# Kernel optimization log

Measured on AMD Instinct MI355X. Metric: run time of the kernel, lower is better.

## Reference

```python
import jax, jax.numpy as jnp
import numpy as np
from jax import lax

SEQ_LEN = 12
E = 64        # embedding_dim
HD = 128      # h_dim
G = 32        # number of scenes (seq_start_end rows)
P = 32        # pedestrians per scene
B = G * P     # total batch
BOT = 1024    # bottleneck_dim
MLP = 1024    # mlp_dim
BN_S = 1.0 / np.sqrt(1.0 + 1e-5)  # eval BatchNorm1d with running mean 0 / var 1


def setup_inputs():
    key = jax.random.key(0)
    ks = jax.random.split(key, 32)
    r = lambda k, s, sc=0.1: (jax.random.normal(k, s, jnp.float32) * sc)
    starts = np.arange(G, dtype=np.int32) * P
    sse = jnp.asarray(np.stack([starts, starts + P], 1))
    return {
        'last_pos': r(ks[0], (B, 2), 1.0),
        'last_pos_rel': r(ks[1], (B, 2), 1.0),
        'h0': r(ks[2], (1, B, HD), 1.0),
        'c0': r(ks[3], (1, B, HD), 1.0),
        'vx': r(ks[4], (8, B), 1.0),
        'vy': r(ks[5], (8, B), 1.0),
        'agent_type': jax.random.uniform(ks[6], (8, B, 1), jnp.float32),
        'seq_start_end': sse,
        # decoder params
        'W_sp': r(ks[7], (2, E)), 'b_sp': r(ks[8], (E,)),
        'W_ih': r(ks[9], (E, 4 * HD)), 'W_hh': r(ks[10], (HD, 4 * HD)),
        'b_ih': r(ks[11], (4 * HD,)), 'b_hh': r(ks[12], (4 * HD,)),
        'W_h2p': r(ks[13], (HD, 2)), 'b_h2p': r(ks[14], (2,)),
        # AttenPoolNet params
        'Wp_sp': r(ks[15], (2, E)), 'bp_sp': r(ks[16], (E,)),
        'Wp_vel': r(ks[17], (2, E)), 'bp_vel': r(ks[18], (E,)),
        'Wp_at': r(ks[19], (6, E)), 'bp_at': r(ks[20], (E,)),
        'Wa1': r(ks[21], (E, MLP)), 'ba1': r(ks[22], (MLP,)),
        'Wa2': r(ks[23], (MLP, 1)), 'ba2': r(ks[24], (1,)),
        'Wm1': r(ks[25], (E + HD, 512)), 'bm1': r(ks[26], (512,)),
        'Wm2': r(ks[27], (512, BOT)), 'bm2': r(ks[28], (BOT,)),
        # decoder post-pool mlp: [h+bottleneck, mlp_dim, h]
        'Wd1': r(ks[29], (HD + BOT, MLP)), 'bd1': r(ks[30], (MLP,)),
        'Wd2': r(ks[31], (MLP, HD)), 'bd2': jnp.zeros((HD,), jnp.float32),
    }


def _bnrelu(x):
    # make_mlp: Linear -> BatchNorm1d (eval, mean 0 / var 1) -> ReLU
    return jax.nn.relu(x * BN_S)


def reference(last_pos, last_pos_rel, h0, c0, vx, vy, agent_type, seq_start_end,
              W_sp, b_sp, W_ih, W_hh, b_ih, b_hh, W_h2p, b_h2p,
              Wp_sp, bp_sp, Wp_vel, bp_vel, Wp_at, bp_at,
              Wa1, ba1, Wa2, ba2, Wm1, bm1, Wm2, bm2,
              Wd1, bd1, Wd2, bd2):
    g = seq_start_end.shape[0]
    p = last_pos.shape[0] // g

    at0 = agent_type[0].reshape(g, p, 1)               # agent_type[0,:,:] per group
    at_rep = jnp.repeat(at0, 6, axis=-1)               # .repeat(num_ped, 6) width expansion
    at_emb = at_rep @ Wp_at + bp_at                    # (g,p,E), index j (tiled over i)
    vel = jnp.stack([vx[-1], vy[-1]], -1).reshape(g, p, 2)
    _vel_emb = vel @ Wp_vel + bp_vel                   # computed in source, unused downstream

    def pool(h2d, pos):
        Hh = h2d.reshape(g, p, HD)
        pg = pos.reshape(g, p, 2)
        # rel[s,i,j] = pos[s,j] - pos[s,i]
        rel = pg[:, None, :, :] - pg[:, :, None, :]
        rel_emb = rel @ Wp_sp + bp_sp                  # (g,p,p,E)
        a = _bnrelu(rel_emb @ Wa1 + ba1)               # (g,p,p,MLP)
        s = _bnrelu(a @ Wa2 + ba2)                     # (g,p,p,1)
        w = jax.nn.softmax(s, axis=-1)                 # torch softmax(dim=1) over size-1 axis -> ones
        base = jnp.concatenate([Hh, at_emb], -1)       # (g,p,192), index j
        wt = base[:, None, :, :] * (0.05 * w)          # (g,p,p,192)
        m = _bnrelu(wt @ Wm1 + bm1)
        m = _bnrelu(m @ Wm2 + bm2)                     # (g,p,p,BOT)
        return m.max(axis=2).reshape(g * p, BOT)       # max over j per tile index i

    def lstm(x, h, c):
        gates = x @ W_ih + h @ W_hh + b_ih + b_hh
        i, f, gg, o = jnp.split(gates, 4, axis=-1)
        c = jax.nn.sigmoid(f) * c + jax.nn.sigmoid(i) * jnp.tanh(gg)
        h = jax.nn.sigmoid(o) * jnp.tanh(c)
        return h, c

    def step(carry, _):
        lp, di, h, c = carry
        h, c = lstm(di, h, c)
        rel = h @ W_h2p + b_h2p
        cur = rel + lp
        ph = pool(h, cur)
        dh = _bnrelu(jnp.concatenate([h, ph], -1) @ Wd1 + bd1)
        dh = _bnrelu(dh @ Wd2 + bd2)
        di = rel @ W_sp + b_sp
        return (cur, di, dh, c), rel

    init = (last_pos, last_pos_rel @ W_sp + b_sp, h0[0], c0[0])
    (lp, di, h, c), rels = lax.scan(step, init, None, length=SEQ_LEN)
    return rels, h[None]  # (seq_len,B,2), (1,B,HD)
```

## Files before the change

### kernel.cpp

```cpp
#include <hip/hip_runtime.h>
#include <math.h>

#define BN_SF 0.9999950000374997f

typedef __attribute__((ext_vector_type(8))) short short8v;
typedef __attribute__((ext_vector_type(4))) float float4v;

__device__ __forceinline__ float sigm(float x) { return 1.0f / (1.0f + expf(-x)); }

__device__ __forceinline__ short f2bf(float x) {
    unsigned u = __builtin_bit_cast(unsigned, x);
    unsigned r = (u + 0x7fffu + ((u >> 16) & 1u)) >> 16;
    return (short)r;
}
__device__ __forceinline__ float bf2f(short h) {
    unsigned u = ((unsigned)(unsigned short)h) << 16;
    return __builtin_bit_cast(float, u);
}

template <int K, int N>
__device__ __forceinline__ void cvtB8(const float* __restrict__ src, short* __restrict__ dst,
                                      float scale, int g) {
    const int KCN = K >> 5;
    int ntg = g / (KCN * 64);
    int rem = g - ntg * (KCN * 64);
    int kc = rem >> 6, lane = rem & 63;
    int n = ntg * 16 + (lane & 15);
    int k0 = kc * 32 + ((lane >> 4) << 3);
    short8v v;
#pragma unroll
    for (int j = 0; j < 8; ++j) v[j] = f2bf(scale * src[(size_t)(k0 + j) * N + n]);
    *(short8v*)(dst + (size_t)g * 8) = v;
}

struct SetupP {
    const float *Wm2, *Wd1, *Wd2, *Wm1, *Wih, *Whh, *Wpat, *bpat, *bm1;
    const float *lpr, *Wsp, *bsp, *c0;
    short *Wm2s, *Wd1f, *Wd2f, *Wm1f, *WgHi, *WgLo;
    float *uv, *di, *cbuf;
};

__global__ __launch_bounds__(256) void k_setup(SetupP p) {
    int gt = blockIdx.x * 256 + threadIdx.x;
    int stride = gridDim.x * 256;
    for (int g = gt; g < 512 * 1024 / 8; g += stride)  cvtB8<512, 1024>(p.Wm2, p.Wm2s, 1.f, g);
    for (int g = gt; g < 1152 * 1024 / 8; g += stride) cvtB8<1152, 1024>(p.Wd1, p.Wd1f, 1.f, g);
    for (int g = gt; g < 1024 * 128 / 8; g += stride)  cvtB8<1024, 128>(p.Wd2, p.Wd2f, 1.f, g);
    for (int g = gt; g < 128 * 512 / 8; g += stride)   cvtB8<128, 512>(p.Wm1, p.Wm1f, 0.05f, g);
    for (int g = gt; g < 192 * 512 / 8; g += stride) {
        int ntg = g / (6 * 64);
        int rem = g - ntg * (6 * 64);
        int kc = rem >> 6, lane = rem & 63;
        int n = ntg * 16 + (lane & 15);
        int k0 = kc * 32 + ((lane >> 4) << 3);
        short8v vh, vl;
#pragma unroll
        for (int j = 0; j < 8; ++j) {
            int k = k0 + j;
            float v = (k < 64) ? p.Wih[(size_t)k * 512 + n] : p.Whh[(size_t)(k - 64) * 512 + n];
            short hi = f2bf(v);
            vh[j] = hi; vl[j] = f2bf(v - bf2f(hi));
        }
        *(short8v*)(p.WgHi + (size_t)g * 8) = vh;
        *(short8v*)(p.WgLo + (size_t)g * 8) = vl;
    }
    for (int i = gt; i < 1024 * 64; i += stride) {
        int r = i >> 6, c = i & 63;
        p.di[i] = p.lpr[r * 2] * p.Wsp[c] + p.lpr[r * 2 + 1] * p.Wsp[64 + c] + p.bsp[c];
    }
    for (int i = gt; i < 1024 * 128; i += stride) p.cbuf[i] = p.c0[i];
    if (blockIdx.x == 0) {
        __shared__ float rw[64];
        int t = threadIdx.x;
        if (t < 64) { float s = 0.f; for (int k = 0; k < 6; ++k) s += p.Wpat[k * 64 + t]; rw[t] = s; }
        __syncthreads();
        for (int c = t; c < 512; c += 256) {
            float u = 0.f, v = 0.f;
            for (int e = 0; e < 64; ++e) {
                float wg = p.Wm1[(128 + e) * 512 + c];
                u += rw[e] * wg; v += p.bpat[e] * wg;
            }
            p.uv[c] = 0.05f * u; p.uv[512 + c] = 0.05f * v + p.bm1[c];
        }
    }
}

__global__ __launch_bounds__(512, 4) void k_step(
    const short* __restrict__ WgHi, const short* __restrict__ WgLo,
    const short* __restrict__ Wm1f, const short* __restrict__ Wd2f,
    const short* __restrict__ Wd1f,
    const float* __restrict__ bih, const float* __restrict__ bhh,
    const float* __restrict__ Whp, const float* __restrict__ bhp,
    const float* __restrict__ Wsp, const float* __restrict__ bsp,
    const float* __restrict__ bd1, const float* __restrict__ bd2,
    const float* __restrict__ at0, const float* __restrict__ uv,
    const float* __restrict__ h0,
    const float* __restrict__ phwp, const short* __restrict__ hf_in, int first,
    float* __restrict__ cbuf, float* __restrict__ di,
    short* __restrict__ hf_out, short* __restrict__ m1s,
    float* __restrict__ outrel) {
    __shared__ float sgu[16 * 512];
    __shared__ float sh[16][128];
    __shared__ float sdi[16][64];
    __shared__ float phws[1024];
    __shared__ short xfh[6 * 512];
    __shared__ short xfl[6 * 512];
    __shared__ short xm[4 * 512];
    __shared__ float sat[16];
    __shared__ float srel[16][2];
    short* dh1L = (short*)sgu;
    float* sg = sgu;

    int t = threadIdx.x, b = blockIdx.x;
    int l = t & 63, w = t >> 6;
    int s = b >> 1, mt = b & 1, r0 = b * 16;
    int rbase = (l >> 4) << 2;

    for (int i = t; i < 16 * 64; i += 512) sdi[i >> 6][i & 63] = di[r0 * 64 + i];
    if (t < 16) sat[t] = at0[r0 + t];

    if (first) {
        for (int i = t; i < 16 * 128; i += 512) sh[i >> 7][i & 127] = h0[r0 * 128 + i];
        __syncthreads();
    } else {
        for (int i = t; i < 1024; i += 512) {
            float v = bd1[i];
#pragma unroll
            for (int ct = 0; ct < 8; ++ct) v += phwp[(size_t)s * 8192 + ct * 1024 + i];
            phws[i] = v;
        }
        __syncthreads();
        short8v Ah[4];
#pragma unroll
        for (int kc = 0; kc < 4; ++kc)
            Ah[kc] = *(const short8v*)(hf_in + (size_t)b * 2048 + kc * 512 + l * 8);
#pragma unroll 1
        for (int q2 = 0; q2 < 4; ++q2) {
            short8v B[2][4];
#pragma unroll
            for (int qq = 0; qq < 2; ++qq)
#pragma unroll
                for (int kc = 0; kc < 4; ++kc)
                    B[qq][kc] = *(const short8v*)(Wd1f + (size_t)(w * 8 + q2 * 2 + qq) * 18432 + kc * 512 + l * 8);
            float4v acc2[2];
#pragma unroll
            for (int qq = 0; qq < 2; ++qq) {
                int col = (w * 8 + q2 * 2 + qq) * 16 + (l & 15);
                float pv = phws[col];
                acc2[qq] = (float4v){pv, pv, pv, pv};
            }
#pragma unroll
            for (int kc = 0; kc < 4; ++kc)
#pragma unroll
                for (int qq = 0; qq < 2; ++qq)
                    acc2[qq] = __builtin_amdgcn_mfma_f32_16x16x32_bf16(Ah[kc], B[qq][kc], acc2[qq], 0, 0, 0);
#pragma unroll
            for (int qq = 0; qq < 2; ++qq) {
                int col = (w * 8 + q2 * 2 + qq) * 16 + (l & 15);
                int kcD = col >> 5, jD = col & 7, lD = ((col & 31) >> 3) << 4;
#pragma unroll
                for (int r = 0; r < 4; ++r) {
                    float v = fmaxf(BN_SF * acc2[qq][r], 0.f);
                    dh1L[kcD * 512 + (rbase + r + lD) * 8 + jD] = f2bf(v);
                }
            }
        }
        __syncthreads();
        float4v hacc = {0.f, 0.f, 0.f, 0.f};
        const short* ap = dh1L + l * 8;
        const short* bp = Wd2f + (size_t)w * 16384 + l * 8;
#pragma unroll 1
        for (int kt = 0; kt < 4; ++kt) {
            short8v B[8], A[8];
#pragma unroll
            for (int kk = 0; kk < 8; ++kk) B[kk] = *(const short8v*)(bp + (kt * 8 + kk) * 512);
#pragma unroll
            for (int kk = 0; kk < 8; ++kk) A[kk] = *(const short8v*)(ap + (kt * 8 + kk) * 512);
#pragma unroll
            for (int kk = 0; kk < 8; ++kk)
                hacc = __builtin_amdgcn_mfma_f32_16x16x32_bf16(A[kk], B[kk], hacc, 0, 0, 0);
        }
        int col = w * 16 + (l & 15);
        float bb2 = bd2[col];
        __syncthreads();
#pragma unroll
        for (int r = 0; r < 4; ++r)
            sh[rbase + r][col] = fmaxf(BN_SF * (hacc[r] + bb2), 0.f);
        __syncthreads();
    }

    for (int i = t; i < 6 * 512; i += 512) {
        int pos = i & 511, kc = i >> 9;
        int ll = pos >> 3, j = pos & 7;
        int row = ll & 15, k = kc * 32 + ((ll >> 4) << 3) + j;
        float v = (k < 64) ? sdi[row][k] : sh[row][k - 64];
        short hi = f2bf(v);
        xfh[i] = hi;
        xfl[i] = f2bf(v - bf2f(hi));
    }
    __syncthreads();

    {
        float4v ga[4] = {{0,0,0,0},{0,0,0,0},{0,0,0,0},{0,0,0,0}};
#pragma unroll 1
        for (int kt = 0; kt < 3; ++kt) {
            short8v BH[2][4], BL[2][4], AH[2], AL[2];
#pragma unroll
            for (int kk = 0; kk < 2; ++kk) {
                int kc = kt * 2 + kk;
#pragma unroll
                for (int q = 0; q < 4; ++q) {
                    int nf = w * 4 + q;
                    BH[kk][q] = *(const short8v*)(WgHi + (size_t)nf * 3072 + kc * 512 + l * 8);
                    BL[kk][q] = *(const short8v*)(WgLo + (size_t)nf * 3072 + kc * 512 + l * 8);
                }
                AH[kk] = *(const short8v*)(&xfh[kc * 512 + l * 8]);
                AL[kk] = *(const short8v*)(&xfl[kc * 512 + l * 8]);
            }
#pragma unroll
            for (int kk = 0; kk < 2; ++kk)
#pragma unroll
                for (int q = 0; q < 4; ++q) {
                    ga[q] = __builtin_amdgcn_mfma_f32_16x16x32_bf16(AH[kk], BH[kk][q], ga[q], 0, 0, 0);
                    ga[q] = __builtin_amdgcn_mfma_f32_16x16x32_bf16(AH[kk], BL[kk][q], ga[q], 0, 0, 0);
                    ga[q] = __builtin_amdgcn_mfma_f32_16x16x32_bf16(AL[kk], BH[kk][q], ga[q], 0, 0, 0);
                }
        }
#pragma unroll
        for (int q = 0; q < 4; ++q) {
            int col = (w * 4 + q) * 16 + (l & 15);
            float bb = bih[col] + bhh[col];
#pragma unroll
            for (int r = 0; r < 4; ++r)
                sg[(rbase + r) * 512 + col] = ga[q][r] + bb;
        }
    }
    __syncthreads();

    for (int i = t; i < 16 * 128; i += 512) {
        int row = i >> 7, j = i & 127;
        float gi = sg[row * 512 + j], gf = sg[row * 512 + j + 128];
        float gg = sg[row * 512 + j + 256], go = sg[row * 512 + j + 384];
        float cn = sigm(gf) * cbuf[(r0 + row) * 128 + j] + sigm(gi) * tanhf(gg);
        float hn = sigm(go) * tanhf(cn);
        cbuf[(r0 + row) * 128 + j] = cn;
        sh[row][j] = hn;
    }
    __syncthreads();

    if (t < 32) {
        int row = t >> 1, d = t & 1;
        float s2 = bhp[d];
        for (int k = 0; k < 128; ++k) s2 += sh[row][k] * Whp[k * 2 + d];
        srel[row][d] = s2;
        outrel[(r0 + row) * 2 + d] = s2;
    }
    for (int i = t; i < 4 * 512; i += 512) {
        int pos = i & 511, kc = i >> 9;
        int ll = pos >> 3, j = pos & 7;
        int row = ll & 15, k = kc * 32 + ((ll >> 4) << 3) + j;
        short hv = f2bf(sh[row][k]);
        xm[i] = hv;
        hf_out[(size_t)b * 2048 + i] = hv;
    }
    __syncthreads();

    for (int i = t; i < 16 * 64; i += 512) {
        int row = i >> 6, c = i & 63;
        di[(r0 + row) * 64 + c] = srel[row][0] * Wsp[c] + srel[row][1] * Wsp[64 + c] + bsp[c];
    }

    {
        float4v ma[4] = {{0,0,0,0},{0,0,0,0},{0,0,0,0},{0,0,0,0}};
        short8v A[4], B[4][4];
#pragma unroll
        for (int kc = 0; kc < 4; ++kc) {
#pragma unroll
            for (int q = 0; q < 4; ++q)
                B[kc][q] = *(const short8v*)(Wm1f + (size_t)(w * 4 + q) * 2048 + kc * 512 + l * 8);
            A[kc] = *(const short8v*)(&xm[kc * 512 + l * 8]);
        }
#pragma unroll
        for (int kc = 0; kc < 4; ++kc)
#pragma unroll
            for (int q = 0; q < 4; ++q)
                ma[q] = __builtin_amdgcn_mfma_f32_16x16x32_bf16(A[kc], B[kc][q], ma[q], 0, 0, 0);
#pragma unroll
        for (int q = 0; q < 4; ++q) {
            int col = (w * 4 + q) * 16 + (l & 15);
            float uc = uv[col], vc = uv[512 + col];
#pragma unroll
            for (int r = 0; r < 4; ++r) {
                int rowC = rbase + r;
                float m1v = fmaxf(BN_SF * (ma[q][r] + sat[rowC] * uc + vc), 0.f);
                int kcD = col >> 5;
                int laneD = rowC + (((col & 31) >> 3) << 4);
                m1s[(size_t)s * 16384 + kcD * 1024 + mt * 512 + laneD * 8 + (col & 7)] = f2bf(m1v);
            }
        }
    }
}

__global__ __launch_bounds__(512, 4) void k_m2(const short* __restrict__ m1s,
                                               const short* __restrict__ Wm2s,
                                               const short* __restrict__ Wd1f,
                                               const float* __restrict__ bm2,
                                               float* __restrict__ phwp) {
    __shared__ short sphb[128];
    int t = threadIdx.x, l = t & 63, w = t >> 6;
    int s = blockIdx.x >> 3, ct = blockIdx.x & 7;

    {
        int nf = ct * 8 + w;
        const short* ap = m1s + (size_t)s * 16384 + l * 8;
        const short* bp = Wm2s + (size_t)nf * 8192 + l * 8;
        float4v acc0 = {0,0,0,0}, acc1 = {0,0,0,0};
#pragma unroll 1
        for (int kt = 0; kt < 4; ++kt) {
            short8v A0[4], A1[4], B[4];
#pragma unroll
            for (int kk = 0; kk < 4; ++kk) {
                int kc = kt * 4 + kk;
                B[kk] = *(const short8v*)(bp + kc * 512);
                A0[kk] = *(const short8v*)(ap + kc * 1024);
                A1[kk] = *(const short8v*)(ap + kc * 1024 + 512);
            }
#pragma unroll
            for (int kk = 0; kk < 4; ++kk) {
                acc0 = __builtin_amdgcn_mfma_f32_16x16x32_bf16(A0[kk], B[kk], acc0, 0, 0, 0);
                acc1 = __builtin_amdgcn_mfma_f32_16x16x32_bf16(A1[kk], B[kk], acc1, 0, 0, 0);
            }
        }
        float m = acc0[0];
#pragma unroll
        for (int ri = 1; ri < 4; ++ri) m = fmaxf(m, acc0[ri]);
#pragma unroll
        for (int ri = 0; ri < 4; ++ri) m = fmaxf(m, acc1[ri]);
        m = fmaxf(m, __shfl_xor(m, 16, 64));
        m = fmaxf(m, __shfl_xor(m, 32, 64));
        if (l < 16) {
            int col = nf * 16 + l;
            sphb[w * 16 + l] = f2bf(fmaxf(BN_SF * (m + bm2[col]), 0.f));
        }
    }
    __syncthreads();

    {
        short8v Ap[4];
#pragma unroll
        for (int kk = 0; kk < 4; ++kk)
            Ap[kk] = *(const short8v*)(sphb + kk * 32 + ((l >> 4) << 3));
#pragma unroll 1
        for (int q2 = 0; q2 < 4; ++q2) {
            short8v B[2][4];
#pragma unroll
            for (int qq = 0; qq < 2; ++qq)
#pragma unroll
                for (int kk = 0; kk < 4; ++kk)
                    B[qq][kk] = *(const short8v*)(Wd1f + (size_t)(w * 8 + q2 * 2 + qq) * 18432
                                                  + (size_t)(4 + ct * 4 + kk) * 512 + l * 8);
            float4v acc2[2] = {{0,0,0,0},{0,0,0,0}};
#pragma unroll
            for (int kk = 0; kk < 4; ++kk)
#pragma unroll
                for (int qq = 0; qq < 2; ++qq)
                    acc2[qq] = __builtin_amdgcn_mfma_f32_16x16x32_bf16(Ap[kk], B[qq][kk], acc2[qq], 0, 0, 0);
            if (l < 16) {
#pragma unroll
                for (int qq = 0; qq < 2; ++qq) {
                    int nf_p = w * 8 + q2 * 2 + qq;
                    phwp[(size_t)s * 8192 + ct * 1024 + nf_p * 16 + l] = acc2[qq][0];
                }
            }
        }
    }
}

__global__ __launch_bounds__(512, 4) void k_hfin(const short* __restrict__ Wd2f,
                                                 const short* __restrict__ Wd1f,
                                                 const float* __restrict__ bd1,
                                                 const float* __restrict__ bd2,
                                                 const float* __restrict__ phwp,
                                                 const short* __restrict__ hf,
                                                 float* __restrict__ outh) {
    __shared__ float phws[1024];
    __shared__ short dh1L[16384];
    int t = threadIdx.x, b = blockIdx.x;
    int l = t & 63, w = t >> 6;
    int s = b >> 1, rbase = (l >> 4) << 2;

    for (int i = t; i < 1024; i += 512) {
        float v = bd1[i];
#pragma unroll
        for (int ct = 0; ct < 8; ++ct) v += phwp[(size_t)s * 8192 + ct * 1024 + i];
        phws[i] = v;
    }
    __syncthreads();
    short8v Ah[4];
#pragma unroll
    for (int kc = 0; kc < 4; ++kc)
        Ah[kc] = *(const short8v*)(hf + (size_t)b * 2048 + kc * 512 + l * 8);
#pragma unroll 1
    for (int q2 = 0; q2 < 4; ++q2) {
        short8v B[2][4];
#pragma unroll
        for (int qq = 0; qq < 2; ++qq)
#pragma unroll
            for (int kc = 0; kc < 4; ++kc)
                B[qq][kc] = *(const short8v*)(Wd1f + (size_t)(w * 8 + q2 * 2 + qq) * 18432 + kc * 512 + l * 8);
        float4v acc2[2];
#pragma unroll
        for (int qq = 0; qq < 2; ++qq) {
            int col = (w * 8 + q2 * 2 + qq) * 16 + (l & 15);
            float pv = phws[col];
            acc2[qq] = (float4v){pv, pv, pv, pv};
        }
#pragma unroll
        for (int kc = 0; kc < 4; ++kc)
#pragma unroll
            for (int qq = 0; qq < 2; ++qq)
                acc2[qq] = __builtin_amdgcn_mfma_f32_16x16x32_bf16(Ah[kc], B[qq][kc], acc2[qq], 0, 0, 0);
#pragma unroll
        for (int qq = 0; qq < 2; ++qq) {
            int col = (w * 8 + q2 * 2 + qq) * 16 + (l & 15);
            int kcD = col >> 5, jD = col & 7, lD = ((col & 31) >> 3) << 4;
#pragma unroll
            for (int r = 0; r < 4; ++r) {
                float v = fmaxf(BN_SF * acc2[qq][r], 0.f);
                dh1L[kcD * 512 + (rbase + r + lD) * 8 + jD] = f2bf(v);
            }
        }
    }
    __syncthreads();
    float4v hacc = {0.f, 0.f, 0.f, 0.f};
    const short* ap = dh1L + l * 8;
    const short* bp = Wd2f + (size_t)w * 16384 + l * 8;
#pragma unroll 1
    for (int kt = 0; kt < 4; ++kt) {
        short8v B[8], A[8];
#pragma unroll
        for (int kk = 0; kk < 8; ++kk) B[kk] = *(const short8v*)(bp + (kt * 8 + kk) * 512);
#pragma unroll
        for (int kk = 0; kk < 8; ++kk) A[kk] = *(const short8v*)(ap + (kt * 8 + kk) * 512);
#pragma unroll
        for (int kk = 0; kk < 8; ++kk)
            hacc = __builtin_amdgcn_mfma_f32_16x16x32_bf16(A[kk], B[kk], hacc, 0, 0, 0);
    }
    int col = w * 16 + (l & 15);
    float bb2 = bd2[col];
#pragma unroll
    for (int r = 0; r < 4; ++r)
        outh[(b * 16 + rbase + r) * 128 + col] = fmaxf(BN_SF * (hacc[r] + bb2), 0.f);
}

extern "C" void kernel_launch(void* const* d_in, const int* in_sizes, int n_in,
                              void* d_out, int out_size, void* d_ws, size_t ws_size,
                              hipStream_t stream) {
    const float* last_pos_rel = (const float*)d_in[1];
    const float* h0           = (const float*)d_in[2];
    const float* c0           = (const float*)d_in[3];
    const float* agent_type   = (const float*)d_in[6];
    const float* W_sp  = (const float*)d_in[8];
    const float* b_sp  = (const float*)d_in[9];
    const float* W_ih  = (const float*)d_in[10];
    const float* W_hh  = (const float*)d_in[11];
    const float* b_ih  = (const float*)d_in[12];
    const float* b_hh  = (const float*)d_in[13];
    const float* W_h2p = (const float*)d_in[14];
    const float* b_h2p = (const float*)d_in[15];
    const float* Wp_at = (const float*)d_in[20];
    const float* bp_at = (const float*)d_in[21];
    const float* Wm1   = (const float*)d_in[26];
    const float* bm1   = (const float*)d_in[27];
    const float* Wm2   = (const float*)d_in[28];
    const float* bm2   = (const float*)d_in[29];
    const float* Wd1   = (const float*)d_in[30];
    const float* bd1   = (const float*)d_in[31];
    const float* Wd2   = (const float*)d_in[32];
    const float* bd2   = (const float*)d_in[33];
    float* out = (float*)d_out;

    float* ws   = (float*)d_ws;
    float* uv   = ws;
    float* di   = uv + 1024;
    float* cbuf = di + 65536;
    float* phwp = cbuf + 131072;
    short* hf   = (short*)(phwp + 262144);
    short* m1s  = hf + 131072;
    short* Wm2s = m1s + 524288;
    short* Wd1f = Wm2s + 524288;
    short* Wd2f = Wd1f + 1179648;
    short* Wm1f = Wd2f + 131072;
    short* WgHi = Wm1f + 65536;
    short* WgLo = WgHi + 98304;

    SetupP sp;
    sp.Wm2 = Wm2; sp.Wd1 = Wd1; sp.Wd2 = Wd2; sp.Wm1 = Wm1;
    sp.Wih = W_ih; sp.Whh = W_hh; sp.Wpat = Wp_at; sp.bpat = bp_at; sp.bm1 = bm1;
    sp.lpr = last_pos_rel; sp.Wsp = W_sp; sp.bsp = b_sp; sp.c0 = c0;
    sp.Wm2s = Wm2s; sp.Wd1f = Wd1f; sp.Wd2f = Wd2f;
    sp.Wm1f = Wm1f; sp.WgHi = WgHi; sp.WgLo = WgLo;
    sp.uv = uv; sp.di = di; sp.cbuf = cbuf;

    k_setup<<<2048, 256, 0, stream>>>(sp);

    for (int t = 0; t < 12; ++t) {
        k_step<<<64, 512, 0, stream>>>(WgHi, WgLo, Wm1f, Wd2f, Wd1f,
                                       b_ih, b_hh, W_h2p, b_h2p, W_sp, b_sp,
                                       bd1, bd2, agent_type, uv, h0,
                                       phwp, hf, (t == 0) ? 1 : 0,
                                       cbuf, di, hf, m1s, out + (size_t)t * 2048);
        k_m2<<<256, 512, 0, stream>>>(m1s, Wm2s, Wd1f, bm2, phwp);
    }
    k_hfin<<<64, 512, 0, stream>>>(Wd2f, Wd1f, bd1, bd2, phwp, hf, out + 24576);
}
```

Measured before the change: 372.9 us.

## Move h@Wd1 and di@W_ih projections from serial step kernel into wide m2 kernel

The h-part of the decoder Wd1 matmul and the input-side LSTM gate projection (di@W_ih plus biases) move out of the 64-block k_step kernel into the 256-block k_m2 kernel. There they are computed ahead of time and stored as bf16 hwf and fp32 gdip buffers. k_step then only adds the pooled contribution and applies BN/ReLU, so its critical path shrinks at the cost of extra global traffic and more work in k_m2. The first step computes di@W_ih directly in scalar code, and setup is merged into one grid-stride loop with vectorized c0 copy.

```diff
diff --git a/kernel.cpp b/kernel.cpp
--- a/kernel.cpp
+++ b/kernel.cpp
@@ -34,41 +34,40 @@
 }
 
 struct SetupP {
-    const float *Wm2, *Wd1, *Wd2, *Wm1, *Wih, *Whh, *Wpat, *bpat, *bm1;
-    const float *lpr, *Wsp, *bsp, *c0;
+    const float *Wm2, *Wd1, *Wd2, *Wm1, *Wih, *Whh, *Wpat, *bpat, *bm1, *c0;
     short *Wm2s, *Wd1f, *Wd2f, *Wm1f, *WgHi, *WgLo;
-    float *uv, *di, *cbuf;
+    float *uv, *cbuf;
 };
 
 __global__ __launch_bounds__(256) void k_setup(SetupP p) {
     int gt = blockIdx.x * 256 + threadIdx.x;
     int stride = gridDim.x * 256;
-    for (int g = gt; g < 512 * 1024 / 8; g += stride)  cvtB8<512, 1024>(p.Wm2, p.Wm2s, 1.f, g);
-    for (int g = gt; g < 1152 * 1024 / 8; g += stride) cvtB8<1152, 1024>(p.Wd1, p.Wd1f, 1.f, g);
-    for (int g = gt; g < 1024 * 128 / 8; g += stride)  cvtB8<1024, 128>(p.Wd2, p.Wd2f, 1.f, g);
-    for (int g = gt; g < 128 * 512 / 8; g += stride)   cvtB8<128, 512>(p.Wm1, p.Wm1f, 0.05f, g);
-    for (int g = gt; g < 192 * 512 / 8; g += stride) {
-        int ntg = g / (6 * 64);
-        int rem = g - ntg * (6 * 64);
-        int kc = rem >> 6, lane = rem & 63;
-        int n = ntg * 16 + (lane & 15);
-        int k0 = kc * 32 + ((lane >> 4) << 3);
-        short8v vh, vl;
-#pragma unroll
-        for (int j = 0; j < 8; ++j) {
-            int k = k0 + j;
-            float v = (k < 64) ? p.Wih[(size_t)k * 512 + n] : p.Whh[(size_t)(k - 64) * 512 + n];
-            short hi = f2bf(v);
-            vh[j] = hi; vl[j] = f2bf(v - bf2f(hi));
-        }
-        *(short8v*)(p.WgHi + (size_t)g * 8) = vh;
-        *(short8v*)(p.WgLo + (size_t)g * 8) = vl;
-    }
-    for (int i = gt; i < 1024 * 64; i += stride) {
-        int r = i >> 6, c = i & 63;
-        p.di[i] = p.lpr[r * 2] * p.Wsp[c] + p.lpr[r * 2 + 1] * p.Wsp[64 + c] + p.bsp[c];
-    }
-    for (int i = gt; i < 1024 * 128; i += stride) p.cbuf[i] = p.c0[i];
+    for (int g = gt; g < 249856; g += stride) {
+        if (g < 65536) cvtB8<512, 1024>(p.Wm2, p.Wm2s, 1.f, g);
+        else if (g < 212992) cvtB8<1152, 1024>(p.Wd1, p.Wd1f, 1.f, g - 65536);
+        else if (g < 229376) cvtB8<1024, 128>(p.Wd2, p.Wd2f, 1.f, g - 212992);
+        else if (g < 237568) cvtB8<128, 512>(p.Wm1, p.Wm1f, 0.05f, g - 229376);
+        else {
+            int gg = g - 237568;
+            int ntg = gg / (6 * 64);
+            int rem = gg - ntg * (6 * 64);
+            int kc = rem >> 6, lane = rem & 63;
+            int n = ntg * 16 + (lane & 15);
+            int k0 = kc * 32 + ((lane >> 4) << 3);
+            short8v vh, vl;
+#pragma unroll
+            for (int j = 0; j < 8; ++j) {
+                int k = k0 + j;
+                float v = (k < 64) ? p.Wih[(size_t)k * 512 + n] : p.Whh[(size_t)(k - 64) * 512 + n];
+                short hi = f2bf(v);
+                vh[j] = hi; vl[j] = f2bf(v - bf2f(hi));
+            }
+            *(short8v*)(p.WgHi + (size_t)gg * 8) = vh;
+            *(short8v*)(p.WgLo + (size_t)gg * 8) = vl;
+        }
+    }
+    for (int i = gt; i < 32768; i += stride)
+        ((float4*)p.cbuf)[i] = ((const float4*)p.c0)[i];
     if (blockIdx.x == 0) {
         __shared__ float rw[64];
         int t = threadIdx.x;
@@ -88,24 +87,25 @@
 __global__ __launch_bounds__(512, 4) void k_step(
     const short* __restrict__ WgHi, const short* __restrict__ WgLo,
     const short* __restrict__ Wm1f, const short* __restrict__ Wd2f,
-    const short* __restrict__ Wd1f,
-    const float* __restrict__ bih, const float* __restrict__ bhh,
+    const float* __restrict__ Wih,
     const float* __restrict__ Whp, const float* __restrict__ bhp,
     const float* __restrict__ Wsp, const float* __restrict__ bsp,
+    const float* __restrict__ bih, const float* __restrict__ bhh,
     const float* __restrict__ bd1, const float* __restrict__ bd2,
     const float* __restrict__ at0, const float* __restrict__ uv,
-    const float* __restrict__ h0,
-    const float* __restrict__ phwp, const short* __restrict__ hf_in, int first,
-    float* __restrict__ cbuf, float* __restrict__ di,
-    short* __restrict__ hf_out, short* __restrict__ m1s,
-    float* __restrict__ outrel) {
+    const float* __restrict__ h0, const float* __restrict__ lpr,
+    const float* __restrict__ phwp, const short* __restrict__ hwf,
+    const float* __restrict__ gdip, int first,
+    float* __restrict__ cbuf, short* __restrict__ hf_out,
+    short* __restrict__ difh, short* __restrict__ difl,
+    short* __restrict__ m1s, float* __restrict__ outrel) {
     __shared__ float sgu[16 * 512];
     __shared__ float sh[16][128];
-    __shared__ float sdi[16][64];
     __shared__ float phws[1024];
-    __shared__ short xfh[6 * 512];
-    __shared__ short xfl[6 * 512];
+    __shared__ short xfh[4 * 512];
+    __shared__ short xfl[4 * 512];
     __shared__ short xm[4 * 512];
+    __shared__ float sdi0[16][64];
     __shared__ float sat[16];
     __shared__ float srel[16][2];
     short* dh1L = (short*)sgu;
@@ -116,11 +116,14 @@
     int s = b >> 1, mt = b & 1, r0 = b * 16;
     int rbase = (l >> 4) << 2;
 
-    for (int i = t; i < 16 * 64; i += 512) sdi[i >> 6][i & 63] = di[r0 * 64 + i];
     if (t < 16) sat[t] = at0[r0 + t];
 
     if (first) {
         for (int i = t; i < 16 * 128; i += 512) sh[i >> 7][i & 127] = h0[r0 * 128 + i];
+        for (int i = t; i < 16 * 64; i += 512) {
+            int row = i >> 6, k = i & 63;
+            sdi0[row][k] = lpr[(r0 + row) * 2] * Wsp[k] + lpr[(r0 + row) * 2 + 1] * Wsp[64 + k] + bsp[k];
+        }
         __syncthreads();
     } else {
         for (int i = t; i < 1024; i += 512) {
@@ -130,40 +133,15 @@
             phws[i] = v;
         }
         __syncthreads();
-        short8v Ah[4];
-#pragma unroll
-        for (int kc = 0; kc < 4; ++kc)
-            Ah[kc] = *(const short8v*)(hf_in + (size_t)b * 2048 + kc * 512 + l * 8);
-#pragma unroll 1
-        for (int q2 = 0; q2 < 4; ++q2) {
-            short8v B[2][4];
-#pragma unroll
-            for (int qq = 0; qq < 2; ++qq)
-#pragma unroll
-                for (int kc = 0; kc < 4; ++kc)
-                    B[qq][kc] = *(const short8v*)(Wd1f + (size_t)(w * 8 + q2 * 2 + qq) * 18432 + kc * 512 + l * 8);
-            float4v acc2[2];
-#pragma unroll
-            for (int qq = 0; qq < 2; ++qq) {
-                int col = (w * 8 + q2 * 2 + qq) * 16 + (l & 15);
-                float pv = phws[col];
-                acc2[qq] = (float4v){pv, pv, pv, pv};
-            }
-#pragma unroll
-            for (int kc = 0; kc < 4; ++kc)
-#pragma unroll
-                for (int qq = 0; qq < 2; ++qq)
-                    acc2[qq] = __builtin_amdgcn_mfma_f32_16x16x32_bf16(Ah[kc], B[qq][kc], acc2[qq], 0, 0, 0);
-#pragma unroll
-            for (int qq = 0; qq < 2; ++qq) {
-                int col = (w * 8 + q2 * 2 + qq) * 16 + (l & 15);
-                int kcD = col >> 5, jD = col & 7, lD = ((col & 31) >> 3) << 4;
-#pragma unroll
-                for (int r = 0; r < 4; ++r) {
-                    float v = fmaxf(BN_SF * acc2[qq][r], 0.f);
-                    dh1L[kcD * 512 + (rbase + r + lD) * 8 + jD] = f2bf(v);
-                }
-            }
+        for (int g = t; g < 2048; g += 512) {
+            int kc = g >> 6, ll = g & 63;
+            int colbase = kc * 32 + ((ll >> 4) << 3);
+            short8v hv = *(const short8v*)(hwf + (size_t)b * 16384 + g * 8);
+            short8v o;
+#pragma unroll
+            for (int j = 0; j < 8; ++j)
+                o[j] = f2bf(fmaxf(BN_SF * (bf2f(hv[j]) + phws[colbase + j]), 0.f));
+            *(short8v*)(dh1L + g * 8) = o;
         }
         __syncthreads();
         float4v hacc = {0.f, 0.f, 0.f, 0.f};
@@ -189,11 +167,11 @@
         __syncthreads();
     }
 
-    for (int i = t; i < 6 * 512; i += 512) {
+    for (int i = t; i < 4 * 512; i += 512) {
         int pos = i & 511, kc = i >> 9;
         int ll = pos >> 3, j = pos & 7;
-        int row = ll & 15, k = kc * 32 + ((ll >> 4) << 3) + j;
-        float v = (k < 64) ? sdi[row][k] : sh[row][k - 64];
+        int row = ll & 15, kh = kc * 32 + ((ll >> 4) << 3) + j;
+        float v = sh[row][kh];
         short hi = f2bf(v);
         xfh[i] = hi;
         xfl[i] = f2bf(v - bf2f(hi));
@@ -201,21 +179,40 @@
     __syncthreads();
 
     {
-        float4v ga[4] = {{0,0,0,0},{0,0,0,0},{0,0,0,0},{0,0,0,0}};
+        float4v ga[4];
+#pragma unroll
+        for (int q = 0; q < 4; ++q) {
+            int col = (w * 4 + q) * 16 + (l & 15);
+            if (first) {
+                float a0 = bih[col] + bhh[col];
+                float acc[4] = {a0, a0, a0, a0};
+                for (int k = 0; k < 64; ++k) {
+                    float wv = Wih[(size_t)k * 512 + col];
+#pragma unroll
+                    for (int r = 0; r < 4; ++r) acc[r] += sdi0[rbase + r][k] * wv;
+                }
+#pragma unroll
+                for (int r = 0; r < 4; ++r) ga[q][r] = acc[r];
+            } else {
+#pragma unroll
+                for (int r = 0; r < 4; ++r)
+                    ga[q][r] = gdip[(size_t)((s * 2 + mt) * 16 + rbase + r) * 512 + col];
+            }
+        }
 #pragma unroll 1
-        for (int kt = 0; kt < 3; ++kt) {
+        for (int kt = 0; kt < 2; ++kt) {
             short8v BH[2][4], BL[2][4], AH[2], AL[2];
 #pragma unroll
             for (int kk = 0; kk < 2; ++kk) {
-                int kc = kt * 2 + kk;
+                int kcx = kt * 2 + kk;
 #pragma unroll
                 for (int q = 0; q < 4; ++q) {
                     int nf = w * 4 + q;
-                    BH[kk][q] = *(const short8v*)(WgHi + (size_t)nf * 3072 + kc * 512 + l * 8);
-                    BL[kk][q] = *(const short8v*)(WgLo + (size_t)nf * 3072 + kc * 512 + l * 8);
+                    BH[kk][q] = *(const short8v*)(WgHi + (size_t)nf * 3072 + (2 + kcx) * 512 + l * 8);
+                    BL[kk][q] = *(const short8v*)(WgLo + (size_t)nf * 3072 + (2 + kcx) * 512 + l * 8);
                 }
-                AH[kk] = *(const short8v*)(&xfh[kc * 512 + l * 8]);
-                AL[kk] = *(const short8v*)(&xfl[kc * 512 + l * 8]);
+                AH[kk] = *(const short8v*)(&xfh[kcx * 512 + l * 8]);
+                AL[kk] = *(const short8v*)(&xfl[kcx * 512 + l * 8]);
             }
 #pragma unroll
             for (int kk = 0; kk < 2; ++kk)
@@ -229,10 +226,9 @@
 #pragma unroll
         for (int q = 0; q < 4; ++q) {
             int col = (w * 4 + q) * 16 + (l & 15);
-            float bb = bih[col] + bhh[col];
 #pragma unroll
             for (int r = 0; r < 4; ++r)
-                sg[(rbase + r) * 512 + col] = ga[q][r] + bb;
+                sg[(rbase + r) * 512 + col] = ga[q][r];
         }
     }
     __syncthreads();
@@ -265,9 +261,14 @@
     }
     __syncthreads();
 
-    for (int i = t; i < 16 * 64; i += 512) {
-        int row = i >> 6, c = i & 63;
-        di[(r0 + row) * 64 + c] = srel[row][0] * Wsp[c] + srel[row][1] * Wsp[64 + c] + bsp[c];
+    for (int i = t; i < 1024; i += 512) {
+        int pos = i & 511, kc = i >> 9;
+        int ll = pos >> 3, j = pos & 7;
+        int row = ll & 15, k = kc * 32 + ((ll >> 4) << 3) + j;
+        float dv = srel[row][0] * Wsp[k] + srel[row][1] * Wsp[64 + k] + bsp[k];
+        short hi = f2bf(dv);
+        difh[(size_t)b * 1024 + i] = hi;
+        difl[(size_t)b * 1024 + i] = f2bf(dv - bf2f(hi));
     }
 
     {
@@ -301,14 +302,17 @@
     }
 }
 
-__global__ __launch_bounds__(512, 4) void k_m2(const short* __restrict__ m1s,
-                                               const short* __restrict__ Wm2s,
-                                               const short* __restrict__ Wd1f,
-                                               const float* __restrict__ bm2,
-                                               float* __restrict__ phwp) {
+__global__ __launch_bounds__(512, 4) void k_m2(
+    const short* __restrict__ m1s, const short* __restrict__ Wm2s,
+    const short* __restrict__ Wd1f,
+    const short* __restrict__ WgHi, const short* __restrict__ WgLo,
+    const float* __restrict__ bm2, const float* __restrict__ bih, const float* __restrict__ bhh,
+    const short* __restrict__ hf, const short* __restrict__ difh, const short* __restrict__ difl,
+    float* __restrict__ phwp, short* __restrict__ hwf, float* __restrict__ gdip) {
     __shared__ short sphb[128];
     int t = threadIdx.x, l = t & 63, w = t >> 6;
     int s = blockIdx.x >> 3, ct = blockIdx.x & 7;
+    int rbase = (l >> 4) << 2;
 
     {
         int nf = ct * 8 + w;
@@ -343,6 +347,51 @@
             sphb[w * 16 + l] = f2bf(fmaxf(BN_SF * (m + bm2[col]), 0.f));
         }
     }
+
+    {
+        int nf = ct * 8 + w;
+        short8v Bh[4];
+#pragma unroll
+        for (int kc = 0; kc < 4; ++kc)
+            Bh[kc] = *(const short8v*)(Wd1f + (size_t)nf * 18432 + kc * 512 + l * 8);
+        int col = nf * 16 + (l & 15);
+        int kcD = col >> 5, jD = col & 7, lD = ((col & 31) >> 3) << 4;
+#pragma unroll
+        for (int m2i = 0; m2i < 2; ++m2i) {
+            short8v Ah[4];
+#pragma unroll
+            for (int kc = 0; kc < 4; ++kc)
+                Ah[kc] = *(const short8v*)(hf + (size_t)(s * 2 + m2i) * 2048 + kc * 512 + l * 8);
+            float4v hacc = {0.f, 0.f, 0.f, 0.f};
+#pragma unroll
+            for (int kc = 0; kc < 4; ++kc)
+                hacc = __builtin_amdgcn_mfma_f32_16x16x32_bf16(Ah[kc], Bh[kc], hacc, 0, 0, 0);
+#pragma unroll
+            for (int r = 0; r < 4; ++r)
+                hwf[(size_t)(s * 2 + m2i) * 16384 + kcD * 512 + (rbase + r + lD) * 8 + jD] = f2bf(hacc[r]);
+        }
+    }
+
+    {
+        int m2i = w >> 2, q = w & 3;
+        int nfg = ct * 4 + q;
+        float4v g = {0.f, 0.f, 0.f, 0.f};
+#pragma unroll
+        for (int kc = 0; kc < 2; ++kc) {
+            short8v AH = *(const short8v*)(difh + (size_t)(s * 2 + m2i) * 1024 + kc * 512 + l * 8);
+            short8v AL = *(const short8v*)(difl + (size_t)(s * 2 + m2i) * 1024 + kc * 512 + l * 8);
+            short8v BH = *(const short8v*)(WgHi + (size_t)nfg * 3072 + kc * 512 + l * 8);
+            short8v BL = *(const short8v*)(WgLo + (size_t)nfg * 3072 + kc * 512 + l * 8);
+            g = __builtin_amdgcn_mfma_f32_16x16x32_bf16(AH, BH, g, 0, 0, 0);
+            g = __builtin_amdgcn_mfma_f32_16x16x32_bf16(AH, BL, g, 0, 0, 0);
+            g = __builtin_amdgcn_mfma_f32_16x16x32_bf16(AL, BH, g, 0, 0, 0);
+        }
+        int col = nfg * 16 + (l & 15);
+        float bb = bih[col] + bhh[col];
+#pragma unroll
+        for (int r = 0; r < 4; ++r)
+            gdip[(size_t)((s * 2 + m2i) * 16 + rbase + r) * 512 + col] = g[r] + bb;
+    }
     __syncthreads();
 
     {
@@ -377,11 +426,10 @@
 }
 
 __global__ __launch_bounds__(512, 4) void k_hfin(const short* __restrict__ Wd2f,
-                                                 const short* __restrict__ Wd1f,
                                                  const float* __restrict__ bd1,
                                                  const float* __restrict__ bd2,
                                                  const float* __restrict__ phwp,
-                                                 const short* __restrict__ hf,
+                                                 const short* __restrict__ hwf,
                                                  float* __restrict__ outh) {
     __shared__ float phws[1024];
     __shared__ short dh1L[16384];
@@ -396,40 +444,15 @@
         phws[i] = v;
     }
     __syncthreads();
-    short8v Ah[4];
-#pragma unroll
-    for (int kc = 0; kc < 4; ++kc)
-        Ah[kc] = *(const short8v*)(hf + (size_t)b * 2048 + kc * 512 + l * 8);
-#pragma unroll 1
-    for (int q2 = 0; q2 < 4; ++q2) {
-        short8v B[2][4];
-#pragma unroll
-        for (int qq = 0; qq < 2; ++qq)
-#pragma unroll
-            for (int kc = 0; kc < 4; ++kc)
-                B[qq][kc] = *(const short8v*)(Wd1f + (size_t)(w * 8 + q2 * 2 + qq) * 18432 + kc * 512 + l * 8);
-        float4v acc2[2];
-#pragma unroll
-        for (int qq = 0; qq < 2; ++qq) {
-            int col = (w * 8 + q2 * 2 + qq) * 16 + (l & 15);
-            float pv = phws[col];
-            acc2[qq] = (float4v){pv, pv, pv, pv};
-        }
-#pragma unroll
-        for (int kc = 0; kc < 4; ++kc)
-#pragma unroll
-            for (int qq = 0; qq < 2; ++qq)
-                acc2[qq] = __builtin_amdgcn_mfma_f32_16x16x32_bf16(Ah[kc], B[qq][kc], acc2[qq], 0, 0, 0);
-#pragma unroll
-        for (int qq = 0; qq < 2; ++qq) {
-            int col = (w * 8 + q2 * 2 + qq) * 16 + (l & 15);
-            int kcD = col >> 5, jD = col & 7, lD = ((col & 31) >> 3) << 4;
-#pragma unroll
-            for (int r = 0; r < 4; ++r) {
-                float v = fmaxf(BN_SF * acc2[qq][r], 0.f);
-                dh1L[kcD * 512 + (rbase + r + lD) * 8 + jD] = f2bf(v);
-            }
-        }
+    for (int g = t; g < 2048; g += 512) {
+        int kc = g >> 6, ll = g & 63;
+        int colbase = kc * 32 + ((ll >> 4) << 3);
+        short8v hv = *(const short8v*)(hwf + (size_t)b * 16384 + g * 8);
+        short8v o;
+#pragma unroll
+        for (int j = 0; j < 8; ++j)
+            o[j] = f2bf(fmaxf(BN_SF * (bf2f(hv[j]) + phws[colbase + j]), 0.f));
+        *(short8v*)(dh1L + g * 8) = o;
     }
     __syncthreads();
     float4v hacc = {0.f, 0.f, 0.f, 0.f};
@@ -456,10 +479,10 @@
 extern "C" void kernel_launch(void* const* d_in, const int* in_sizes, int n_in,
                               void* d_out, int out_size, void* d_ws, size_t ws_size,
                               hipStream_t stream) {
-    const float* last_pos_rel = (const float*)d_in[1];
-    const float* h0           = (const float*)d_in[2];
-    const float* c0           = (const float*)d_in[3];
-    const float* agent_type   = (const float*)d_in[6];
+    const float* lpr   = (const float*)d_in[1];
+    const float* h0    = (const float*)d_in[2];
+    const float* c0    = (const float*)d_in[3];
+    const float* at0   = (const float*)d_in[6];
     const float* W_sp  = (const float*)d_in[8];
     const float* b_sp  = (const float*)d_in[9];
     const float* W_ih  = (const float*)d_in[10];
@@ -480,37 +503,43 @@
     const float* bd2   = (const float*)d_in[33];
     float* out = (float*)d_out;
 
-    float* ws   = (float*)d_ws;
-    float* uv   = ws;
-    float* di   = uv + 1024;
-    float* cbuf = di + 65536;
-    float* phwp = cbuf + 131072;
-    short* hf   = (short*)(phwp + 262144);
-    short* m1s  = hf + 131072;
-    short* Wm2s = m1s + 524288;
-    short* Wd1f = Wm2s + 524288;
-    short* Wd2f = Wd1f + 1179648;
-    short* Wm1f = Wd2f + 131072;
-    short* WgHi = Wm1f + 65536;
-    short* WgLo = WgHi + 98304;
+    float* ws    = (float*)d_ws;
+    float* uv    = ws;
+    float* cbuf  = uv + 1024;
+    float* phwp  = cbuf + 131072;
+    float* gdip  = phwp + 262144;
+    short* hf    = (short*)(gdip + 524288);
+    short* difh  = hf + 131072;
+    short* difl  = difh + 65536;
+    short* m1s   = difl + 65536;
+    short* hwf   = m1s + 524288;
+    short* Wm2s  = hwf + 1048576;
+    short* Wd1f  = Wm2s + 524288;
+    short* Wd2f  = Wd1f + 1179648;
+    short* Wm1f  = Wd2f + 131072;
+    short* WgHi  = Wm1f + 65536;
+    short* WgLo  = WgHi + 98304;
 
     SetupP sp;
     sp.Wm2 = Wm2; sp.Wd1 = Wd1; sp.Wd2 = Wd2; sp.Wm1 = Wm1;
     sp.Wih = W_ih; sp.Whh = W_hh; sp.Wpat = Wp_at; sp.bpat = bp_at; sp.bm1 = bm1;
-    sp.lpr = last_pos_rel; sp.Wsp = W_sp; sp.bsp = b_sp; sp.c0 = c0;
+    sp.c0 = c0;
     sp.Wm2s = Wm2s; sp.Wd1f = Wd1f; sp.Wd2f = Wd2f;
     sp.Wm1f = Wm1f; sp.WgHi = WgHi; sp.WgLo = WgLo;
-    sp.uv = uv; sp.di = di; sp.cbuf = cbuf;
-
-    k_setup<<<2048, 256, 0, stream>>>(sp);
+    sp.uv = uv; sp.cbuf = cbuf;
+
+    k_setup<<<1024, 256, 0, stream>>>(sp);
 
     for (int t = 0; t < 12; ++t) {
-        k_step<<<64, 512, 0, stream>>>(WgHi, WgLo, Wm1f, Wd2f, Wd1f,
-                                       b_ih, b_hh, W_h2p, b_h2p, W_sp, b_sp,
-                                       bd1, bd2, agent_type, uv, h0,
-                                       phwp, hf, (t == 0) ? 1 : 0,
-                                       cbuf, di, hf, m1s, out + (size_t)t * 2048);
-        k_m2<<<256, 512, 0, stream>>>(m1s, Wm2s, Wd1f, bm2, phwp);
-    }
-    k_hfin<<<64, 512, 0, stream>>>(Wd2f, Wd1f, bd1, bd2, phwp, hf, out + 24576);
-}
+        k_step<<<64, 512, 0, stream>>>(WgHi, WgLo, Wm1f, Wd2f, W_ih,
+                                       W_h2p, b_h2p, W_sp, b_sp, b_ih, b_hh,
+                                       bd1, bd2, at0, uv, h0, lpr,
+                                       phwp, hwf, gdip, (t == 0) ? 1 : 0,
+                                       cbuf, hf, difh, difl, m1s,
+                                       out + (size_t)t * 2048);
+        k_m2<<<256, 512, 0, stream>>>(m1s, Wm2s, Wd1f, WgHi, WgLo,
+                                      bm2, b_ih, b_hh, hf, difh, difl,
+                                      phwp, hwf, gdip);
+    }
+    k_hfin<<<64, 512, 0, stream>>>(Wd2f, bd1, bd2, phwp, hwf, out + 24576);
+}
```

Measured after the change: 405.2 us. 1.09x slower.
